# Kernel tuning notes

Measured on AMD Instinct MI355X. Metric: run time of the kernel, lower is better.

## Reference

```python
import jax, jax.numpy as jnp
import numpy as np

D_MODEL = 768
D_STATE = 16
D_CONV = 4
EXPAND = 2
D_INNER = D_MODEL * EXPAND  # 1536
BATCH = 2
SEQ = 2048


def _silu(v):
    return v * jax.nn.sigmoid(v)


def setup_inputs() -> dict:
    key = jax.random.key(0)
    ks = jax.random.split(key, 8)
    s = 0.02
    x = jax.random.normal(ks[0], (BATCH, SEQ, D_MODEL), jnp.float32)
    in_proj_w = jax.random.normal(ks[1], (2 * D_INNER, D_MODEL), jnp.float32) * s
    conv_w = jax.random.normal(ks[2], (D_INNER, 1, D_CONV), jnp.float32) * 0.2
    conv_b = jax.random.normal(ks[3], (D_INNER,), jnp.float32) * 0.02
    x_proj_w = jax.random.normal(ks[4], (2 * D_STATE + D_INNER, D_INNER), jnp.float32) * s
    dt_proj_w = jax.random.normal(ks[5], (D_INNER, D_INNER), jnp.float32) * s
    dt_proj_b = jax.random.normal(ks[6], (D_INNER,), jnp.float32) * 0.02
    A_log = jnp.log(jnp.broadcast_to(jnp.arange(1, D_STATE + 1, dtype=jnp.float32), (D_INNER, D_STATE)))
    D_param = jnp.ones((D_INNER,), jnp.float32)
    out_proj_w = jax.random.normal(ks[7], (D_MODEL, D_INNER), jnp.float32) * s
    return dict(x=x, in_proj_w=in_proj_w, conv_w=conv_w, conv_b=conv_b,
                x_proj_w=x_proj_w, dt_proj_w=dt_proj_w, dt_proj_b=dt_proj_b,
                A_log=A_log, D_param=D_param, out_proj_w=out_proj_w)


def reference(x, in_proj_w, conv_w, conv_b, x_proj_w, dt_proj_w, dt_proj_b,
              A_log, D_param, out_proj_w):
    B, L, _ = x.shape
    # input projection -> (x_in, z)
    xz = jnp.einsum('bld,ed->ble', x, in_proj_w)          # (B, L, 2*d_inner)
    x_in, z = xz[..., :D_INNER], xz[..., D_INNER:]
    # causal depthwise conv1d (torch pad=d_conv-1 both sides then truncate to L == left pad)
    x_pad = jnp.pad(x_in, ((0, 0), (D_CONV - 1, 0), (0, 0)))
    lhs = x_pad.transpose(0, 2, 1)                        # (B, d_inner, L+pad)
    conv = jax.lax.conv_general_dilated(lhs, conv_w, (1,), 'VALID',
                                        feature_group_count=D_INNER)
    x_conv = _silu(conv.transpose(0, 2, 1) + conv_b)      # (B, L, d_inner)
    # ssm parameterization
    x_dbl = jnp.einsum('bld,ed->ble', x_conv, x_proj_w)
    delta_raw = x_dbl[..., :D_INNER]
    B_ssm = x_dbl[..., D_INNER:D_INNER + D_STATE]         # (B, L, N)
    C_ssm = x_dbl[..., D_INNER + D_STATE:]                # (B, L, N)
    delta = jax.nn.softplus(jnp.einsum('bld,ed->ble', delta_raw, dt_proj_w) + dt_proj_b)
    A = -jnp.exp(A_log)                                   # (d_inner, N)
    dA = jnp.exp(jnp.einsum('bld,dn->bldn', delta, A))    # (B, L, d_inner, N)
    dB_u = jnp.einsum('bld,bln,bld->bldn', delta, B_ssm, x_conv)

    def step(h, inp):
        dA_t, dBu_t, C_t = inp                            # (B,d,N),(B,d,N),(B,N)
        h = dA_t * h + dBu_t
        y_t = jnp.einsum('bdn,bn->bd', h, C_t)
        return h, y_t

    h0 = jnp.zeros((B, D_INNER, D_STATE), x.dtype)
    _, ys = jax.lax.scan(step, h0, (dA.transpose(1, 0, 2, 3),
                                    dB_u.transpose(1, 0, 2, 3),
                                    C_ssm.transpose(1, 0, 2)))
    y = ys.transpose(1, 0, 2) + x_conv * D_param          # (B, L, d_inner)
    y = y * _silu(z)
    return jnp.einsum('bld,ed->ble', y, out_proj_w)       # (B, L, d_model)
```

## Files before the change

kernel.cpp:

```cpp
#include <hip/hip_runtime.h>
#include <hip/hip_fp16.h>
#include <cstdint>

#define D_MODEL 768
#define D_STATE 16
#define D_CONV  4
#define D_INNER 1536
#define BATCH   2
#define SEQ     2048
#define M_ROWS  (BATCH*SEQ)
#define XZ_LD   (2*D_INNER)
#define XDBL_N  (D_INNER + 2*D_STATE)
#define WFULL_R 1664
#define NCHUNK  128
#define CH      16
#define DGRP    (D_INNER/256)

typedef __attribute__((ext_vector_type(8))) _Float16 f16x8;
typedef __attribute__((ext_vector_type(4))) float f32x4;
typedef __attribute__((ext_vector_type(8))) ushort ushort8v;
typedef const __attribute__((address_space(1))) void* as1cv;
typedef __attribute__((address_space(3))) void* as3v;

#define LOG2E 1.44269504088896f

__device__ __forceinline__ ushort f2h(float f) { return __half_as_ushort(__float2half(f)); }
__device__ __forceinline__ float h2f(ushort u) { return __half2float(__ushort_as_half(u)); }
__device__ __forceinline__ float silu_f(float v) {
    return v / (1.f + __builtin_exp2f(-v * LOG2E));
}
__device__ __forceinline__ float softplus_f(float t) {
    float e = __builtin_exp2f(-fabsf(t) * LOG2E);
    return fmaxf(t, 0.f) + __log2f(1.f + e) * 0.69314718056f;
}

__global__ __launch_bounds__(256) void prep_convh(
    const float* __restrict__ s0, ushort* __restrict__ d0,
    const float* __restrict__ s1, ushort* __restrict__ d1,
    const float* __restrict__ s2, ushort* __restrict__ d2,
    const float* __restrict__ s3, ushort* __restrict__ d3)
{
    int b = blockIdx.x;
    const float* s; ushort* d; int i;
    if (b < 3072)      { s = s0; d = d0; i = b * 256 + threadIdx.x; }
    else if (b < 5376) { s = s1; d = d1; i = (b - 3072) * 256 + threadIdx.x; }
    else if (b < 7680) { s = s2; d = d2; i = (b - 5376) * 256 + threadIdx.x; }
    else               { s = s3; d = d3; i = (b - 7680) * 256 + threadIdx.x; }
    float4 v = ((const float4*)s)[i];
    ushort4 h;
    h.x = f2h(v.x); h.y = f2h(v.y); h.z = f2h(v.z); h.w = f2h(v.w);
    ((ushort4*)d)[i] = h;
}

__global__ __launch_bounds__(256) void transpose_h(const float* __restrict__ src,
                                                   ushort* __restrict__ dst) {
    __shared__ ushort t[64][65];
    const int bx = blockIdx.x * 64;
    const int by = blockIdx.y * 64;
    const int c = threadIdx.x & 63, r0 = threadIdx.x >> 6;
    #pragma unroll
    for (int i = 0; i < 16; ++i) {
        int r = r0 + i * 4;
        t[c][r] = f2h(src[(size_t)(by + r) * D_INNER + bx + c]);
    }
    __syncthreads();
    #pragma unroll
    for (int i = 0; i < 16; ++i) {
        int rr = r0 + i * 4;
        dst[(size_t)(bx + rr) * D_INNER + by + c] = t[rr][c];
    }
}

__global__ __launch_bounds__(256) void bc_pad(const float* __restrict__ xpw,
                                              ushort* __restrict__ Wfull,
                                              const float* __restrict__ cw,
                                              float* __restrict__ cwT) {
    int b = blockIdx.x;
    if (b < 768) {
        int i = b * 256 + threadIdx.x;
        int row = 1536 + i / D_INNER, col = i % D_INNER;
        float v = (row < XDBL_N) ? xpw[(size_t)row * D_INNER + col] : 0.f;
        Wfull[(size_t)row * D_INNER + col] = f2h(v);
    } else {
        int i = (b - 768) * 256 + threadIdx.x;
        int tap = i / D_INNER, ch = i % D_INNER;
        cwT[i] = cw[ch * D_CONV + tap];
    }
}

__global__ __launch_bounds__(256) void reduce_add_h(const float* __restrict__ Cp, size_t zstride,
                                                    ushort* __restrict__ dst, int n4) {
    int i = blockIdx.x * 256 + threadIdx.x;
    if (i >= n4) return;
    float4 a = ((const float4*)Cp)[i];
    float4 b = ((const float4*)(Cp + zstride))[i];
    ushort4 h;
    h.x = f2h(a.x + b.x); h.y = f2h(a.y + b.y); h.z = f2h(a.z + b.z); h.w = f2h(a.w + b.w);
    ((ushort4*)dst)[i] = h;
}
__global__ __launch_bounds__(256) void reduce_add_f(const float* __restrict__ Cp, size_t zstride,
                                                    float* __restrict__ dst, int n4) {
    int i = blockIdx.x * 256 + threadIdx.x;
    if (i >= n4) return;
    float4 a = ((const float4*)Cp)[i];
    float4 b = ((const float4*)(Cp + zstride))[i];
    a.x += b.x; a.y += b.y; a.z += b.z; a.w += b.w;
    ((float4*)dst)[i] = a;
}

template<int OM, int NZ>
__global__ __launch_bounds__(256, 2) void gemm_h(
    const ushort* __restrict__ A, const ushort* __restrict__ W,
    const float* __restrict__ bias,
    float* __restrict__ Cf, float* __restrict__ Cf2,
    ushort* __restrict__ Oh, ushort* __restrict__ Oh2,
    int N, int K, size_t zstride)
{
    __shared__ ushort As[2][128*64];
    __shared__ ushort Ws[2][128*64];
    const int tid = threadIdx.x, lane = tid & 63, wave = tid >> 6;
    const int gx = gridDim.x, nwg = gx * gridDim.y;
    const int lid = blockIdx.y * gx + blockIdx.x;
    const int swz = (lid & 7) * (nwg >> 3) + (lid >> 3);
    const int bm = (swz / gx) * 128, bn = (swz % gx) * 128;
    const int wr = wave >> 1, wc = wave & 1;
    const int r15 = lane & 15, q = lane >> 4;
    const int xorv = (lane & 7) << 4;
    f32x4 acc[4][4] = {};

    const int Kp = K / NZ;
    const int kbeg = (NZ > 1) ? blockIdx.z * Kp : 0;

    int sRow[4], sCol[4], sOff[4];
    #pragma unroll
    for (int i = 0; i < 4; ++i) {
        int off = wave*4096 + i*1024 + lane*16;
        int row = off >> 7;
        sRow[i] = row;
        sCol[i] = (off & 127) ^ ((row & 7) << 4);
        sOff[i] = wave*4096 + i*1024;
    }

    auto STAGE = [&](int b, int k0) {
        #pragma unroll
        for (int i = 0; i < 4; ++i) {
            size_t ar = ((size_t)(bm + sRow[i]) * K + kbeg + k0) * 2;
            __builtin_amdgcn_global_load_lds((as1cv)((const char*)A + ar + sCol[i]),
                                             (as3v)((char*)As[b] + sOff[i]), 16, 0, 0);
        }
        #pragma unroll
        for (int i = 0; i < 4; ++i) {
            size_t wr_ = ((size_t)(bn + sRow[i]) * K + kbeg + k0) * 2;
            __builtin_amdgcn_global_load_lds((as1cv)((const char*)W + wr_ + sCol[i]),
                                             (as3v)((char*)Ws[b] + sOff[i]), 16, 0, 0);
        }
    };

    STAGE(0, 0);
    const int nt = Kp / 64;
    for (int t = 0; t < nt; ++t) {
        const int cur = t & 1;
        if (t + 1 < nt) {
            STAGE(cur ^ 1, (t + 1) * 64);
            asm volatile("s_waitcnt vmcnt(8)" ::: "memory");
        } else {
            asm volatile("s_waitcnt vmcnt(0)" ::: "memory");
        }
        __builtin_amdgcn_s_barrier();
        #pragma unroll
        for (int kk = 0; kk < 2; ++kk) {
            const int kb = kk*64 + q*16;
            f16x8 af[4], wf[4];
            #pragma unroll
            for (int m = 0; m < 4; ++m) {
                int row = wr*64 + m*16 + r15;
                af[m] = *(const f16x8*)((const char*)As[cur] + row*128 + (kb ^ xorv));
            }
            #pragma unroll
            for (int n = 0; n < 4; ++n) {
                int row = wc*64 + n*16 + r15;
                wf[n] = *(const f16x8*)((const char*)Ws[cur] + row*128 + (kb ^ xorv));
            }
            #pragma unroll
            for (int m = 0; m < 4; ++m)
                #pragma unroll
                for (int n = 0; n < 4; ++n)
                    acc[m][n] = __builtin_amdgcn_mfma_f32_16x16x32_f16(af[m], wf[n], acc[m][n], 0, 0, 0);
        }
        asm volatile("s_waitcnt lgkmcnt(0)" ::: "memory");
        __builtin_amdgcn_s_barrier();
    }

    #pragma unroll
    for (int m = 0; m < 4; ++m) {
        #pragma unroll
        for (int n = 0; n < 4; ++n) {
            int col = bn + wc*64 + n*16 + r15;
            #pragma unroll
            for (int r = 0; r < 4; ++r) {
                int rowg = bm + wr*64 + m*16 + q*4 + r;
                float v = acc[m][n][r];
                if constexpr (OM == 1) {
                    if (col < D_INNER) Oh[(size_t)rowg * D_INNER + col] = f2h(v);
                    else Oh2[(size_t)rowg * D_INNER + (col - D_INNER)] = f2h(silu_f(v));
                } else if constexpr (OM == 2) {
                    if (col < D_INNER) {
                        Oh[(size_t)rowg * D_INNER + col] = f2h(softplus_f(v + bias[col]));
                    } else if (col < XDBL_N) {
                        Cf2[(size_t)rowg * 32 + (col - D_INNER)] = v;
                    }
                } else {
                    Cf[(size_t)blockIdx.z * zstride + (size_t)rowg * N + col] = v;
                }
            }
        }
    }
}

__global__ __launch_bounds__(256) void conv_silu(
    const ushort* __restrict__ xin,
    const float* __restrict__ cwT,
    const float* __restrict__ cb,
    ushort* __restrict__ xch)
{
    const int t  = blockIdx.x * 256 + threadIdx.x;
    const int d8 = t % (D_INNER / 8);
    const int rc = t / (D_INNER / 8);
    const int l0 = (rc & (SEQ / 4 - 1)) * 4;
    const int row0 = rc * 4;
    const int d  = d8 * 8;

    float w[4][8];
    #pragma unroll
    for (int j = 0; j < 4; ++j) {
        float4 a = *(const float4*)&cwT[j * D_INNER + d];
        float4 b = *(const float4*)&cwT[j * D_INNER + d + 4];
        w[j][0]=a.x; w[j][1]=a.y; w[j][2]=a.z; w[j][3]=a.w;
        w[j][4]=b.x; w[j][5]=b.y; w[j][6]=b.z; w[j][7]=b.w;
    }
    float bias[8];
    {
        float4 a = *(const float4*)&cb[d];
        float4 b = *(const float4*)&cb[d + 4];
        bias[0]=a.x; bias[1]=a.y; bias[2]=a.z; bias[3]=a.w;
        bias[4]=b.x; bias[5]=b.y; bias[6]=b.z; bias[7]=b.w;
    }

    float xw[7][8];
    #pragma unroll
    for (int i = 0; i < 7; ++i) {
        if (l0 + i - 3 >= 0) {
            ushort8v v = *(const ushort8v*)&xin[(size_t)(row0 + i - 3) * D_INNER + d];
            #pragma unroll
            for (int c = 0; c < 8; ++c) xw[i][c] = h2f(v[c]);
        } else {
            #pragma unroll
            for (int c = 0; c < 8; ++c) xw[i][c] = 0.f;
        }
    }

    #pragma unroll
    for (int r = 0; r < 4; ++r) {
        ushort8v o;
        #pragma unroll
        for (int c = 0; c < 8; ++c) {
            float acc = bias[c];
            #pragma unroll
            for (int j = 0; j < 4; ++j)
                acc = fmaf(w[j][c], xw[r + j][c], acc);
            o[c] = f2h(silu_f(acc));
        }
        *(ushort8v*)&xch[(size_t)(row0 + r) * D_INNER + d] = o;
    }
}

__global__ __launch_bounds__(256, 4) void scan_pass1(
    const ushort* __restrict__ delta,
    const float* __restrict__ bc,
    const ushort* __restrict__ xch,
    const float* __restrict__ A_log,
    ushort* __restrict__ Pc, ushort* __restrict__ Hc)
{
    const int blk = blockIdx.x;
    const int dg = blk % DGRP;
    const int c  = (blk / DGRP) % NCHUNK;
    const int b  = blk / (DGRP * NCHUNK);
    const int d  = dg * 256 + threadIdx.x;
    const int row0 = b * SEQ + c * CH;

    float AregL2[D_STATE];
    #pragma unroll
    for (int r = 0; r < 4; ++r) {
        float4 a = *(const float4*)&A_log[d * D_STATE + r * 4];
        AregL2[r*4+0] = -__builtin_exp2f(a.x * LOG2E) * LOG2E;
        AregL2[r*4+1] = -__builtin_exp2f(a.y * LOG2E) * LOG2E;
        AregL2[r*4+2] = -__builtin_exp2f(a.z * LOG2E) * LOG2E;
        AregL2[r*4+3] = -__builtin_exp2f(a.w * LOG2E) * LOG2E;
    }

    float dl[CH], xc[CH];
    #pragma unroll
    for (int j = 0; j < CH; ++j)
        dl[j] = h2f(delta[(size_t)(row0 + j) * D_INNER + d]);
    #pragma unroll
    for (int j = 0; j < CH; ++j)
        xc[j] = h2f(xch[(size_t)(row0 + j) * D_INNER + d]);

    float h[D_STATE] = {};
    float sumdlt = 0.f;
    #pragma unroll
    for (int j = 0; j < CH; ++j) {
        const float dlt = dl[j];
        const float dbx = dlt * xc[j];
        sumdlt += dlt;
        const float* brow = bc + (size_t)(row0 + j) * 32;
        #pragma unroll
        for (int n = 0; n < D_STATE; ++n)
            h[n] = fmaf(__builtin_exp2f(dlt * AregL2[n]), h[n], dbx * brow[n]);
    }

    size_t o = ((size_t)(b * NCHUNK + c) * D_INNER + d) * D_STATE;
    #pragma unroll
    for (int r = 0; r < 2; ++r) {
        ushort8v hv, pv;
        #pragma unroll
        for (int i = 0; i < 8; ++i) {
            hv[i] = f2h(h[r*8 + i]);
            pv[i] = f2h(__builtin_exp2f(AregL2[r*8 + i] * sumdlt));
        }
        ((ushort8v*)(Hc + o))[r] = hv;
        ((ushort8v*)(Pc + o))[r] = pv;
    }
}

__global__ __launch_bounds__(256) void scan_pass2(
    ushort* __restrict__ Pc, const ushort* __restrict__ Hc)
{
    int t = blockIdx.x * 256 + threadIdx.x;
    int b = t / (D_INNER * D_STATE);
    int dn = t % (D_INNER * D_STATE);
    float h = 0.f;
    for (int c = 0; c < NCHUNK; ++c) {
        size_t o = (size_t)(b * NCHUNK + c) * (D_INNER * D_STATE) + dn;
        float P  = h2f(Pc[o]);
        float hc = h2f(Hc[o]);
        Pc[o] = f2h(h);
        h = fmaf(P, h, hc);
    }
}

__global__ __launch_bounds__(256, 4) void scan_pass3(
    const ushort* __restrict__ delta, const float* __restrict__ bc,
    const ushort* __restrict__ xch,
    const ushort* __restrict__ zg,
    const float* __restrict__ A_log, const float* __restrict__ Dpar,
    const ushort* __restrict__ Hin,
    ushort* __restrict__ yh)
{
    const int blk = blockIdx.x;
    const int dg = blk % DGRP;
    const int c  = (blk / DGRP) % NCHUNK;
    const int b  = blk / (DGRP * NCHUNK);
    const int d  = dg * 256 + threadIdx.x;
    const int row0 = b * SEQ + c * CH;

    float AregL2[D_STATE];
    #pragma unroll
    for (int r = 0; r < 4; ++r) {
        float4 a = *(const float4*)&A_log[d * D_STATE + r * 4];
        AregL2[r*4+0] = -__builtin_exp2f(a.x * LOG2E) * LOG2E;
        AregL2[r*4+1] = -__builtin_exp2f(a.y * LOG2E) * LOG2E;
        AregL2[r*4+2] = -__builtin_exp2f(a.z * LOG2E) * LOG2E;
        AregL2[r*4+3] = -__builtin_exp2f(a.w * LOG2E) * LOG2E;
    }
    const float Dv = Dpar[d];

    float dl[CH], xc[CH];
    #pragma unroll
    for (int j = 0; j < CH; ++j)
        dl[j] = h2f(delta[(size_t)(row0 + j) * D_INNER + d]);
    #pragma unroll
    for (int j = 0; j < CH; ++j)
        xc[j] = h2f(xch[(size_t)(row0 + j) * D_INNER + d]);

    float h[D_STATE];
    {
        size_t o = ((size_t)(b * NCHUNK + c) * D_INNER + d) * D_STATE;
        #pragma unroll
        for (int r = 0; r < 2; ++r) {
            ushort8v v = ((const ushort8v*)(Hin + o))[r];
            #pragma unroll
            for (int i = 0; i < 8; ++i) h[r*8 + i] = h2f(v[i]);
        }
    }

    #pragma unroll
    for (int j = 0; j < CH; ++j) {
        const float dlt = dl[j];
        const float dbx = dlt * xc[j];
        const float* brow = bc + (size_t)(row0 + j) * 32;
        #pragma unroll
        for (int n = 0; n < D_STATE; ++n)
            h[n] = fmaf(__builtin_exp2f(dlt * AregL2[n]), h[n], dbx * brow[n]);
        float p0 = 0.f, p1 = 0.f, p2 = 0.f, p3 = 0.f;
        #pragma unroll
        for (int n = 0; n < 4; ++n) {
            p0 = fmaf(h[n],      brow[16 + n],      p0);
            p1 = fmaf(h[4 + n],  brow[16 + 4 + n],  p1);
            p2 = fmaf(h[8 + n],  brow[16 + 8 + n],  p2);
            p3 = fmaf(h[12 + n], brow[16 + 12 + n], p3);
        }
        size_t ro = (size_t)(row0 + j) * D_INNER + d;
        const float gate = h2f(zg[ro]);
        const float y = ((p0 + p1) + (p2 + p3) + xc[j] * Dv) * gate;
        yh[ro] = f2h(y);
    }
}

extern "C" void kernel_launch(void* const* d_in, const int* in_sizes, int n_in,
                              void* d_out, int out_size, void* d_ws, size_t ws_size,
                              hipStream_t stream) {
    const float* x         = (const float*)d_in[0];
    const float* in_proj_w = (const float*)d_in[1];
    const float* conv_w    = (const float*)d_in[2];
    const float* conv_b    = (const float*)d_in[3];
    const float* x_proj_w  = (const float*)d_in[4];
    const float* dt_proj_w = (const float*)d_in[5];
    const float* dt_proj_b = (const float*)d_in[6];
    const float* A_log     = (const float*)d_in[7];
    const float* D_param   = (const float*)d_in[8];
    const float* out_proj_w= (const float*)d_in[9];
    float* out = (float*)d_out;

    ushort* xh = (ushort*)d_out;

    char* p = (char*)d_ws;
    ushort* xin  = (ushort*)p;  p += (size_t)M_ROWS * D_INNER * 2;
    ushort* zg   = (ushort*)p;  p += (size_t)M_ROWS * D_INNER * 2;
    float*  bc   = (float*)p;   p += (size_t)M_ROWS * 32 * 4;
    ushort* xch  = (ushort*)p;  p += (size_t)M_ROWS * D_INNER * 2;
    ushort* yh   = (ushort*)p;  p += (size_t)M_ROWS * D_INNER * 2;
    ushort* inwh = (ushort*)p;  p += (size_t)XZ_LD * D_MODEL * 2;
    ushort* Wfull= (ushort*)p;  p += (size_t)WFULL_R * D_INNER * 2;
    ushort* xpwT = (ushort*)p;  p += (size_t)D_INNER * D_INNER * 2;
    ushort* dtwh = (ushort*)p;  p += (size_t)D_INNER * D_INNER * 2;
    ushort* opwh = (ushort*)p;  p += (size_t)D_MODEL * D_INNER * 2;
    float*  cwT  = (float*)p;   p += (size_t)D_CONV * D_INNER * 4;
    float*  scratch = (float*)p;  p += (size_t)2 * M_ROWS * D_MODEL * 4;

    ushort* delta = xin;
    float*  CpW = scratch;
    ushort* Pc  = (ushort*)scratch;
    ushort* Hc  = Pc + (size_t)BATCH * NCHUNK * D_INNER * D_STATE;
    float*  Cp6 = scratch;

    prep_convh<<<8832, 256, 0, stream>>>(x, xh, in_proj_w, inwh,
                                         dt_proj_w, dtwh, out_proj_w, opwh);
    transpose_h<<<dim3(24,24), 256, 0, stream>>>(x_proj_w, xpwT);
    bc_pad<<<792, 256, 0, stream>>>(x_proj_w, Wfull, conv_w, cwT);

    gemm_h<4,2><<<dim3(12,12,2), 256, 0, stream>>>(
        dtwh, xpwT, nullptr, CpW, nullptr, nullptr, nullptr,
        D_INNER, D_INNER, (size_t)D_INNER * D_INNER);
    reduce_add_h<<<2304, 256, 0, stream>>>(CpW, (size_t)D_INNER * D_INNER, Wfull,
                                           D_INNER * D_INNER / 4);

    gemm_h<1,1><<<dim3(24,32), 256, 0, stream>>>(
        xh, inwh, nullptr, nullptr, nullptr, xin, zg, XZ_LD, D_MODEL, 0);

    conv_silu<<<(M_ROWS / 4) * (D_INNER / 8) / 256, 256, 0, stream>>>(
        xin, cwT, conv_b, xch);

    gemm_h<2,1><<<dim3(13,32), 256, 0, stream>>>(
        xch, Wfull, dt_proj_b, nullptr, bc, delta, nullptr, WFULL_R, D_INNER, 0);

    scan_pass1<<<BATCH * NCHUNK * DGRP, 256, 0, stream>>>(delta, bc, xch, A_log, Pc, Hc);
    scan_pass2<<<(BATCH * D_INNER * D_STATE) / 256, 256, 0, stream>>>(Pc, Hc);
    scan_pass3<<<BATCH * NCHUNK * DGRP, 256, 0, stream>>>(
        delta, bc, xch, zg, A_log, D_param, Pc, yh);

    gemm_h<4,2><<<dim3(6,32,2), 256, 0, stream>>>(
        yh, opwh, nullptr, Cp6, nullptr, nullptr, nullptr,
        D_MODEL, D_INNER, (size_t)M_ROWS * D_MODEL);
    reduce_add_f<<<3072, 256, 0, stream>>>(Cp6, (size_t)M_ROWS * D_MODEL, out,
                                           M_ROWS * D_MODEL / 4);
}
```

Baseline: 242.4 us.

## Triple-buffer GEMM LDS stages with smaller K tile and higher occupancy

Reworks the fp16 MFMA GEMM main loop from a double-buffered 64-wide K tile to a triple-buffered 32-wide K tile. Global-to-LDS loads are now issued two stages ahead, and the loop is manually unrolled by three with adjusted vmcnt waits. The LDS footprint drops, and launch bounds ask for 3 blocks per CU to raise occupancy and hide load latency. In exchange there are twice as many barrier pairs per K and less MFMA work between syncs. The unrolled loop also assumes the K-tile count is a multiple of three.

```diff
diff --git a/kernel.cpp b/kernel.cpp
--- a/kernel.cpp
+++ b/kernel.cpp
@@ -109,15 +109,15 @@
 }
 
 template<int OM, int NZ>
-__global__ __launch_bounds__(256, 2) void gemm_h(
+__global__ __launch_bounds__(256, 3) void gemm_h(
     const ushort* __restrict__ A, const ushort* __restrict__ W,
     const float* __restrict__ bias,
     float* __restrict__ Cf, float* __restrict__ Cf2,
     ushort* __restrict__ Oh, ushort* __restrict__ Oh2,
     int N, int K, size_t zstride)
 {
-    __shared__ ushort As[2][128*64];
-    __shared__ ushort Ws[2][128*64];
+    __shared__ ushort As[3][128*32];
+    __shared__ ushort Ws[3][128*32];
     const int tid = threadIdx.x, lane = tid & 63, wave = tid >> 6;
     const int gx = gridDim.x, nwg = gx * gridDim.y;
     const int lid = blockIdx.y * gx + blockIdx.x;
@@ -125,71 +125,84 @@
     const int bm = (swz / gx) * 128, bn = (swz % gx) * 128;
     const int wr = wave >> 1, wc = wave & 1;
     const int r15 = lane & 15, q = lane >> 4;
-    const int xorv = (lane & 7) << 4;
+    const int kq = q * 16;
+    const int xorv = (lane & 3) << 4;
     f32x4 acc[4][4] = {};
 
     const int Kp = K / NZ;
     const int kbeg = (NZ > 1) ? blockIdx.z * Kp : 0;
 
-    int sRow[4], sCol[4], sOff[4];
-    #pragma unroll
-    for (int i = 0; i < 4; ++i) {
-        int off = wave*4096 + i*1024 + lane*16;
-        int row = off >> 7;
+    int sRow[2], sCol[2], sOff[2];
+    #pragma unroll
+    for (int i = 0; i < 2; ++i) {
+        int off = wave*2048 + i*1024 + lane*16;
+        int row = off >> 6;
         sRow[i] = row;
-        sCol[i] = (off & 127) ^ ((row & 7) << 4);
-        sOff[i] = wave*4096 + i*1024;
+        sCol[i] = (off & 63) ^ ((row & 3) << 4);
+        sOff[i] = wave*2048 + i*1024;
     }
 
     auto STAGE = [&](int b, int k0) {
         #pragma unroll
-        for (int i = 0; i < 4; ++i) {
+        for (int i = 0; i < 2; ++i) {
             size_t ar = ((size_t)(bm + sRow[i]) * K + kbeg + k0) * 2;
             __builtin_amdgcn_global_load_lds((as1cv)((const char*)A + ar + sCol[i]),
                                              (as3v)((char*)As[b] + sOff[i]), 16, 0, 0);
         }
         #pragma unroll
-        for (int i = 0; i < 4; ++i) {
+        for (int i = 0; i < 2; ++i) {
             size_t wr_ = ((size_t)(bn + sRow[i]) * K + kbeg + k0) * 2;
             __builtin_amdgcn_global_load_lds((as1cv)((const char*)W + wr_ + sCol[i]),
                                              (as3v)((char*)Ws[b] + sOff[i]), 16, 0, 0);
         }
     };
 
+    auto COMPUTE = [&](int cur) {
+        f16x8 af[4], wf[4];
+        #pragma unroll
+        for (int m = 0; m < 4; ++m) {
+            int row = wr*64 + m*16 + r15;
+            af[m] = *(const f16x8*)((const char*)As[cur] + row*64 + (kq ^ xorv));
+        }
+        #pragma unroll
+        for (int n = 0; n < 4; ++n) {
+            int row = wc*64 + n*16 + r15;
+            wf[n] = *(const f16x8*)((const char*)Ws[cur] + row*64 + (kq ^ xorv));
+        }
+        #pragma unroll
+        for (int m = 0; m < 4; ++m)
+            #pragma unroll
+            for (int n = 0; n < 4; ++n)
+                acc[m][n] = __builtin_amdgcn_mfma_f32_16x16x32_f16(af[m], wf[n], acc[m][n], 0, 0, 0);
+    };
+
+    const int nt = Kp / 32;
     STAGE(0, 0);
-    const int nt = Kp / 64;
-    for (int t = 0; t < nt; ++t) {
-        const int cur = t & 1;
-        if (t + 1 < nt) {
-            STAGE(cur ^ 1, (t + 1) * 64);
-            asm volatile("s_waitcnt vmcnt(8)" ::: "memory");
-        } else {
-            asm volatile("s_waitcnt vmcnt(0)" ::: "memory");
-        }
-        __builtin_amdgcn_s_barrier();
-        #pragma unroll
-        for (int kk = 0; kk < 2; ++kk) {
-            const int kb = kk*64 + q*16;
-            f16x8 af[4], wf[4];
-            #pragma unroll
-            for (int m = 0; m < 4; ++m) {
-                int row = wr*64 + m*16 + r15;
-                af[m] = *(const f16x8*)((const char*)As[cur] + row*128 + (kb ^ xorv));
-            }
-            #pragma unroll
-            for (int n = 0; n < 4; ++n) {
-                int row = wc*64 + n*16 + r15;
-                wf[n] = *(const f16x8*)((const char*)Ws[cur] + row*128 + (kb ^ xorv));
-            }
-            #pragma unroll
-            for (int m = 0; m < 4; ++m)
-                #pragma unroll
-                for (int n = 0; n < 4; ++n)
-                    acc[m][n] = __builtin_amdgcn_mfma_f32_16x16x32_f16(af[m], wf[n], acc[m][n], 0, 0, 0);
-        }
-        asm volatile("s_waitcnt lgkmcnt(0)" ::: "memory");
-        __builtin_amdgcn_s_barrier();
-    }
+    STAGE(1, 32);
+
+#define BODY(T, CUR)                                                            \
+    {                                                                           \
+        const int t_ = (T);                                                     \
+        if (t_ + 2 < nt) {                                                      \
+            STAGE(((CUR) + 2) % 3, (t_ + 2) * 32);            \
+            asm volatile("s_waitcnt vmcnt(8)" ::: "memory");   \
+        } else if (t_ + 1 < nt) {                                               \
+            asm volatile("s_waitcnt vmcnt(4)" ::: "memory");                    \
+        } else {                                                                \
+            asm volatile("s_waitcnt vmcnt(0)" ::: "memory");                    \
+        }                                                                       \
+        __builtin_amdgcn_s_barrier();                                           \
+        COMPUTE(CUR);                                                           \
+        asm volatile("s_waitcnt lgkmcnt(0)" ::: "memory");                      \
+        __builtin_amdgcn_s_barrier();                                           \
+    }
+
+    for (int t3 = 0; t3 < nt; t3 += 3) {
+        BODY(t3 + 0, 0);
+        BODY(t3 + 1, 1);
+        BODY(t3 + 2, 2);
+    }
+#undef BODY
 
     #pragma unroll
     for (int m = 0; m < 4; ++m) {
```

New measurement: 249.0 us. 1.03x slower.

## Load GEMM weight fragments directly into registers, dropping the LDS weight tile

Applied to the files above, without the earlier changes.

The GEMM no longer stages the weight tile through shared memory. Each wave loads its weight MFMA fragments straight from global memory into registers, double-buffered across two register sets, with the main loop unrolled by two. This halves LDS use so three workgroups can fit per CU (launch bounds raised to 3), and it removes the LDS reads for weights. The costs are higher register pressure, weight reads that are less coalesced and duplicated across waves, and vmcnt waits that depend on exact load counts. A new OM==3 f16 output mode is added, but nothing in the shown code uses it.

```diff
diff --git a/kernel.cpp b/kernel.cpp
--- a/kernel.cpp
+++ b/kernel.cpp
@@ -109,7 +109,7 @@
 }
 
 template<int OM, int NZ>
-__global__ __launch_bounds__(256, 2) void gemm_h(
+__global__ __launch_bounds__(256, 3) void gemm_h(
     const ushort* __restrict__ A, const ushort* __restrict__ W,
     const float* __restrict__ bias,
     float* __restrict__ Cf, float* __restrict__ Cf2,
@@ -117,7 +117,6 @@
     int N, int K, size_t zstride)
 {
     __shared__ ushort As[2][128*64];
-    __shared__ ushort Ws[2][128*64];
     const int tid = threadIdx.x, lane = tid & 63, wave = tid >> 6;
     const int gx = gridDim.x, nwg = gx * gridDim.y;
     const int lid = blockIdx.y * gx + blockIdx.x;
@@ -148,47 +147,65 @@
             __builtin_amdgcn_global_load_lds((as1cv)((const char*)A + ar + sCol[i]),
                                              (as3v)((char*)As[b] + sOff[i]), 16, 0, 0);
         }
-        #pragma unroll
-        for (int i = 0; i < 4; ++i) {
-            size_t wr_ = ((size_t)(bn + sRow[i]) * K + kbeg + k0) * 2;
-            __builtin_amdgcn_global_load_lds((as1cv)((const char*)W + wr_ + sCol[i]),
-                                             (as3v)((char*)Ws[b] + sOff[i]), 16, 0, 0);
-        }
     };
 
-    STAGE(0, 0);
-    const int nt = Kp / 64;
-    for (int t = 0; t < nt; ++t) {
-        const int cur = t & 1;
-        if (t + 1 < nt) {
-            STAGE(cur ^ 1, (t + 1) * 64);
-            asm volatile("s_waitcnt vmcnt(8)" ::: "memory");
-        } else {
-            asm volatile("s_waitcnt vmcnt(0)" ::: "memory");
-        }
-        __builtin_amdgcn_s_barrier();
+    const char* Wbase = (const char*)W + ((size_t)(bn + wc*64 + r15) * K + kbeg) * 2 + q*16;
+
+    f16x8 wfA[8], wfB[8];
+    auto FLOAD = [&](f16x8* wf, int t) {
+        #pragma unroll
+        for (int kk = 0; kk < 2; ++kk)
+            #pragma unroll
+            for (int n = 0; n < 4; ++n)
+                wf[kk*4+n] = *(const f16x8*)(Wbase + (size_t)n*16*K*2 + (size_t)t*128 + kk*64);
+    };
+
+    auto COMPUTE = [&](int cur, const f16x8* wf) {
         #pragma unroll
         for (int kk = 0; kk < 2; ++kk) {
             const int kb = kk*64 + q*16;
-            f16x8 af[4], wf[4];
+            f16x8 af[4];
             #pragma unroll
             for (int m = 0; m < 4; ++m) {
                 int row = wr*64 + m*16 + r15;
                 af[m] = *(const f16x8*)((const char*)As[cur] + row*128 + (kb ^ xorv));
             }
             #pragma unroll
-            for (int n = 0; n < 4; ++n) {
-                int row = wc*64 + n*16 + r15;
-                wf[n] = *(const f16x8*)((const char*)Ws[cur] + row*128 + (kb ^ xorv));
-            }
-            #pragma unroll
             for (int m = 0; m < 4; ++m)
                 #pragma unroll
                 for (int n = 0; n < 4; ++n)
-                    acc[m][n] = __builtin_amdgcn_mfma_f32_16x16x32_f16(af[m], wf[n], acc[m][n], 0, 0, 0);
-        }
+                    acc[m][n] = __builtin_amdgcn_mfma_f32_16x16x32_f16(af[m], wf[kk*4+n], acc[m][n], 0, 0, 0);
+        }
+    };
+
+    const int nt = Kp / 64;
+    FLOAD(wfA, 0);
+    STAGE(0, 0);
+    for (int t2 = 0; t2 < nt; t2 += 2) {
+        if (t2 + 1 < nt) {
+            FLOAD(wfB, t2 + 1);
+            STAGE(1, (t2 + 1) * 64);
+            asm volatile("s_waitcnt vmcnt(12)" ::: "memory");
+        } else {
+            asm volatile("s_waitcnt vmcnt(0)" ::: "memory");
+        }
+        __builtin_amdgcn_s_barrier();
+        COMPUTE(0, wfA);
         asm volatile("s_waitcnt lgkmcnt(0)" ::: "memory");
         __builtin_amdgcn_s_barrier();
+        if (t2 + 1 < nt) {
+            if (t2 + 2 < nt) {
+                FLOAD(wfA, t2 + 2);
+                STAGE(0, (t2 + 2) * 64);
+                asm volatile("s_waitcnt vmcnt(12)" ::: "memory");
+            } else {
+                asm volatile("s_waitcnt vmcnt(0)" ::: "memory");
+            }
+            __builtin_amdgcn_s_barrier();
+            COMPUTE(1, wfB);
+            asm volatile("s_waitcnt lgkmcnt(0)" ::: "memory");
+            __builtin_amdgcn_s_barrier();
+        }
     }
 
     #pragma unroll
@@ -209,6 +226,8 @@
                     } else if (col < XDBL_N) {
                         Cf2[(size_t)rowg * 32 + (col - D_INNER)] = v;
                     }
+                } else if constexpr (OM == 3) {
+                    Oh[(size_t)rowg * D_INNER + col] = f2h(v);
                 } else {
                     Cf[(size_t)blockIdx.z * zstride + (size_t)rowg * N + col] = v;
                 }
```

After: 312.3 us. 1.29x slower.
